# Kernel optimization log

Hardware: AMD Instinct MI355X
Metric: run time of the kernel (lower is better)

Reference implementation:

```python
import jax, jax.numpy as jnp
import numpy as np
import math

# --- config (matches init_kwargs) ---
C = 128          # sphere_channels (multiplicity per l)
LMAX = 2
H = 8            # attention heads
B = 16           # graphs per batch (uniform)
M = 512          # nodes per graph
N = B * M        # 8192 nodes
E = 262144       # edges
D = C * sum(2 * l + 1 for l in range(LMAX + 1))  # 1152
_INV_SQRT_C = 1.0 / math.sqrt(C)


def irreps_linear(x, W):
    """e3nn o3.Linear irreps_node->irreps_node: per-l channel mixing, shared over m.
    x: [N, D], W: [LMAX+1, C, C]."""
    outs = []
    s = 0
    for l in range(LMAX + 1):
        d = 2 * l + 1
        blk = x[:, s:s + C * d].reshape(-1, C, d)          # [N, C, 2l+1]
        y = jnp.einsum('ncm,oc->nom', blk, W[l]) * _INV_SQRT_C
        outs.append(y.reshape(-1, C * d))
        s += C * d
    return jnp.concatenate(outs, axis=1)


def init_edge_rot_mat(edge_vec, edge_rand):
    """Faithful port of init_edge_rot_mat; edge_rand plays the role of rand_like."""
    dist = jnp.sqrt(jnp.sum(edge_vec ** 2, axis=1, keepdims=True))
    nx_ = edge_vec / dist
    e2 = edge_rand - 0.5
    e2 = e2 / jnp.sqrt(jnp.sum(e2 ** 2, axis=1, keepdims=True))
    e2b = jnp.stack([-e2[:, 1], e2[:, 0], e2[:, 2]], axis=1)
    e2c = jnp.stack([e2[:, 0], -e2[:, 2], e2[:, 1]], axis=1)
    dot = lambda a: jnp.abs(jnp.sum(a * nx_, axis=1, keepdims=True))
    vdb, vdc = dot(e2b), dot(e2c)
    e2 = jnp.where(dot(e2) > vdb, e2b, e2)
    e2 = jnp.where(dot(e2) > vdc, e2c, e2)
    nz = jnp.cross(nx_, e2)
    nz = nz / jnp.sqrt(jnp.sum(nz ** 2, axis=1, keepdims=True))
    ny = jnp.cross(nx_, nz)
    ny = ny / jnp.sqrt(jnp.sum(ny ** 2, axis=1, keepdims=True))
    rot_inv = jnp.stack([nz, nx_, -ny], axis=2)  # columns [z, x, -y]
    return jnp.transpose(rot_inv, (0, 2, 1))     # [E, 3, 3]


def setup_inputs() -> dict:
    key = jax.random.key(0)
    ks = jax.random.split(key, 10)
    node_features = jax.random.normal(ks[0], (N, D), dtype=jnp.float32)
    edge_vec = jax.random.normal(ks[1], (E, 3), dtype=jnp.float32)
    edge_rand = jax.random.uniform(ks[2], (E, 3), dtype=jnp.float32)
    edge_index = jax.random.randint(ks[3], (2, E), 0, N, dtype=jnp.int32)
    batch = jnp.repeat(jnp.arange(B, dtype=jnp.int32), M)
    W_q = jax.random.normal(ks[4], (LMAX + 1, C, C), dtype=jnp.float32)
    W_k = jax.random.normal(ks[5], (LMAX + 1, C, C), dtype=jnp.float32)
    W_v = jax.random.normal(ks[6], (LMAX + 1, C, C), dtype=jnp.float32)
    W_o = jax.random.normal(ks[7], (LMAX + 1, C, C), dtype=jnp.float32)
    gamma = jnp.ones((C,), dtype=jnp.float32)
    beta = jnp.zeros((C,), dtype=jnp.float32)
    return dict(node_features=node_features, edge_vec=edge_vec, edge_rand=edge_rand,
                W_q=W_q, W_k=W_k, W_v=W_v, W_o=W_o, gamma=gamma, beta=beta,
                edge_index=edge_index, batch=batch)


def reference(node_features, edge_vec, edge_rand, W_q, W_k, W_v, W_o, gamma, beta,
              edge_index, batch):
    # 1) per-edge rotation matrices (detached in the original)
    rot = jax.lax.stop_gradient(init_edge_rot_mat(edge_vec, edge_rand))

    x = node_features  # [N, D] equivariant irreps features

    # 2) SO2EquivariantGraphAttention: irreps q/k/v, dense per-graph multi-head attn
    q = irreps_linear(x, W_q)
    k = irreps_linear(x, W_k)
    v = irreps_linear(x, W_v)
    hd = D // H
    scale = 1.0 / math.sqrt(hd)
    # to_dense_batch with uniform graph sizes == reshape; mask all-true
    qd = q.reshape(B, M, H, hd).transpose(0, 2, 1, 3)  # [B,H,M,hd]
    kd = k.reshape(B, M, H, hd).transpose(0, 2, 1, 3)
    vd = v.reshape(B, M, H, hd).transpose(0, 2, 1, 3)
    scores = jnp.einsum('bhqd,bhkd->bhqk', qd, kd) * scale
    attn_w = jax.nn.softmax(scores, axis=-1)
    o = jnp.einsum('bhqk,bhkd->bhqd', attn_w, vd)
    o = o.transpose(0, 2, 1, 3).reshape(N, D)
    attn_out = irreps_linear(o, W_o)

    # residual connection
    x = x + attn_out

    # 3) EquivariantLayerNormV2: LayerNorm over l=0 dims only (first C)
    inv = x[:, :C]
    mu = jnp.mean(inv, axis=-1, keepdims=True)
    var = jnp.var(inv, axis=-1, keepdims=True)
    inv = (inv - mu) / jnp.sqrt(var + 1e-5) * gamma + beta

    # 4) S2Activation: SiLU on scalar (l=0) components, identity elsewhere
    inv = jax.nn.silu(inv)
    out = jnp.concatenate([inv, x[:, C:]], axis=1)
    return out, rot
```

## Files before the change

kernel.cpp:

```cpp
#include <hip/hip_runtime.h>
#include <hip/hip_bf16.h>

#define C_CH   128
#define DROW   1152
#define NNODE  8192
#define BATCH  16
#define MSEQ   512
#define NHEAD  8
#define HD     144
#define NEDGE  262144

typedef unsigned short ushort_t;
typedef __attribute__((ext_vector_type(8))) short bf16x8;
typedef __attribute__((ext_vector_type(4))) float f32x4;

__device__ __forceinline__ float ldf(const float* p) { return *p; }
__device__ __forceinline__ float ldf(const __hip_bfloat16* p) { return __bfloat162float(*p); }
__device__ __forceinline__ ushort_t f2bu(float x) {
    __hip_bfloat16 h = __float2bfloat16(x);
    return *reinterpret_cast<ushort_t*>(&h);
}
__device__ __forceinline__ float bu2f(ushort_t u) {
    return __bfloat162float(*reinterpret_cast<__hip_bfloat16*>(&u));
}

#define KP2 136

template<int DL, int NPB, int NZ, int FUSE_LN, typename TX, typename TY>
__global__ __launch_bounds__(256) void lin_mfma(
    const TX* __restrict__ X,
    const float* __restrict__ W0, const float* __restrict__ W1,
    const float* __restrict__ W2,
    TY* __restrict__ Y0, TY* __restrict__ Y1, TY* __restrict__ Y2,
    const float* __restrict__ resid,
    const float* __restrict__ gamma, const float* __restrict__ beta,
    int baseoff)
{
    constexpr int COLS = NPB * DL;
    constexpr int CT   = COLS / 16;
    __shared__ __align__(16) ushort_t Xs[COLS][KP2];
    __shared__ __align__(16) ushort_t Es[COLS][KP2];

    const int tid  = threadIdx.x;
    const int wave = tid >> 6;
    const int lane = tid & 63;
    const int l15  = lane & 15;
    const int quad = lane >> 4;
    const int n0   = blockIdx.x * NPB;

    if constexpr (sizeof(TX) == 4) {
        for (int e4 = tid; e4 < NPB * 32 * DL; e4 += 256) {
            const int nb = e4 / (32 * DL);
            const int rr = (e4 - nb * (32 * DL)) * 4;
            const float4 xv = *reinterpret_cast<const float4*>(
                &X[(size_t)(n0 + nb) * DROW + baseoff + rr]);
            #pragma unroll
            for (int j = 0; j < 4; ++j) {
                const int r = rr + j, c = r / DL, m = r - c * DL;
                Xs[nb * DL + m][c] = f2bu(reinterpret_cast<const float*>(&xv)[j]);
            }
        }
    } else {
        for (int e8 = tid; e8 < NPB * 16 * DL; e8 += 256) {
            const int nb = e8 / (16 * DL);
            const int rr = (e8 - nb * (16 * DL)) * 8;
            const uint4 xv = *reinterpret_cast<const uint4*>(
                &X[(size_t)(n0 + nb) * DROW + baseoff + rr]);
            const ushort_t* xs = reinterpret_cast<const ushort_t*>(&xv);
            #pragma unroll
            for (int j = 0; j < 8; ++j) {
                const int r = rr + j, c = r / DL, m = r - c * DL;
                Xs[nb * DL + m][c] = xs[j];
            }
        }
    }

    const float s = 0.08838834764831845f;

    for (int z = 0; z < NZ; ++z) {
        const float* W = (z == 0) ? W0 : (z == 1 ? W1 : W2);
        TY* Y          = (z == 0) ? Y0 : (z == 1 ? Y1 : Y2);

        bf16x8 aw[2][4];
        #pragma unroll
        for (int ot = 0; ot < 2; ++ot)
            #pragma unroll
            for (int kst = 0; kst < 4; ++kst) {
                const float* wp = &W[(size_t)(32 * wave + 16 * ot + l15) * 128 + kst * 32 + quad * 8];
                const float4 wa = *reinterpret_cast<const float4*>(wp);
                const float4 wb = *reinterpret_cast<const float4*>(wp + 4);
                ushort_t t[8] = {f2bu(wa.x), f2bu(wa.y), f2bu(wa.z), f2bu(wa.w),
                                 f2bu(wb.x), f2bu(wb.y), f2bu(wb.z), f2bu(wb.w)};
                aw[ot][kst] = *reinterpret_cast<const bf16x8*>(t);
            }

        __syncthreads();

        f32x4 acc[CT][2];
        #pragma unroll
        for (int ct = 0; ct < CT; ++ct) {
            acc[ct][0] = (f32x4){0.f, 0.f, 0.f, 0.f};
            acc[ct][1] = (f32x4){0.f, 0.f, 0.f, 0.f};
        }
        #pragma unroll
        for (int kst = 0; kst < 4; ++kst)
            #pragma unroll
            for (int ct = 0; ct < CT; ++ct) {
                const bf16x8 b = *reinterpret_cast<const bf16x8*>(
                    &Xs[ct * 16 + l15][kst * 32 + quad * 8]);
                acc[ct][0] = __builtin_amdgcn_mfma_f32_16x16x32_bf16(aw[0][kst], b, acc[ct][0], 0, 0, 0);
                acc[ct][1] = __builtin_amdgcn_mfma_f32_16x16x32_bf16(aw[1][kst], b, acc[ct][1], 0, 0, 0);
            }

        #pragma unroll
        for (int ct = 0; ct < CT; ++ct)
            #pragma unroll
            for (int ot = 0; ot < 2; ++ot) {
                ushort_t t[4] = {f2bu(acc[ct][ot][0] * s), f2bu(acc[ct][ot][1] * s),
                                 f2bu(acc[ct][ot][2] * s), f2bu(acc[ct][ot][3] * s)};
                *reinterpret_cast<uint2*>(&Es[ct * 16 + l15][32 * wave + 16 * ot + quad * 4]) =
                    *reinterpret_cast<const uint2*>(t);
            }
        __syncthreads();

        if constexpr (FUSE_LN) {
            const int nb = tid >> 2, cc = tid & 3;
            float y[32];
            const float* xr = resid + (size_t)(n0 + nb) * DROW + cc * 32;
            float s1 = 0.f, s2 = 0.f;
            #pragma unroll
            for (int j4 = 0; j4 < 8; ++j4) {
                const float4 rv = *reinterpret_cast<const float4*>(xr + j4 * 4);
                #pragma unroll
                for (int j = 0; j < 4; ++j) {
                    const float v = bu2f(Es[nb][cc * 32 + j4 * 4 + j]) +
                                    reinterpret_cast<const float*>(&rv)[j];
                    y[j4 * 4 + j] = v; s1 += v; s2 += v * v;
                }
            }
            s1 += __shfl_xor(s1, 1); s2 += __shfl_xor(s2, 1);
            s1 += __shfl_xor(s1, 2); s2 += __shfl_xor(s2, 2);
            const float mean = s1 * (1.0f / 128.0f);
            const float var  = s2 * (1.0f / 128.0f) - mean * mean;
            const float rstd = rsqrtf(var + 1e-5f);
            float* op = (float*)Y + (size_t)(n0 + nb) * DROW + cc * 32;
            #pragma unroll
            for (int j4 = 0; j4 < 8; ++j4) {
                float4 ov;
                #pragma unroll
                for (int j = 0; j < 4; ++j) {
                    const int c = cc * 32 + j4 * 4 + j;
                    float t = (y[j4 * 4 + j] - mean) * rstd * gamma[c] + beta[c];
                    reinterpret_cast<float*>(&ov)[j] = t / (1.0f + __expf(-t));
                }
                *reinterpret_cast<float4*>(op + j4 * 4) = ov;
            }
        } else {
            for (int e8 = tid; e8 < COLS * 16; e8 += 256) {
                const int nb = e8 / (16 * DL);
                const int r0 = (e8 - nb * (16 * DL)) * 8;
                const size_t ga = (size_t)(n0 + nb) * DROW + baseoff + r0;
                if constexpr (sizeof(TY) == 2) {
                    ushort_t t[8];
                    #pragma unroll
                    for (int j = 0; j < 8; ++j) {
                        const int r = r0 + j;
                        t[j] = Es[nb * DL + r % DL][r / DL];
                    }
                    *reinterpret_cast<uint4*>(&Y[ga]) = *reinterpret_cast<const uint4*>(t);
                } else {
                    #pragma unroll
                    for (int j4 = 0; j4 < 2; ++j4) {
                        const float4 rv = *reinterpret_cast<const float4*>(&resid[ga + j4 * 4]);
                        float4 ov;
                        #pragma unroll
                        for (int j = 0; j < 4; ++j) {
                            const int r = r0 + j4 * 4 + j;
                            reinterpret_cast<float*>(&ov)[j] =
                                bu2f(Es[nb * DL + r % DL][r / DL]) +
                                reinterpret_cast<const float*>(&rv)[j];
                        }
                        *reinterpret_cast<float4*>(&((float*)Y)[ga + j4 * 4]) = ov;
                    }
                }
            }
        }
    }
}

#define KPAD  168
#define VROWS 160
#define VPAD2 72
#define PPAD  68

__global__ __launch_bounds__(256) void attn_kernel(
    const __hip_bfloat16* __restrict__ Q, const __hip_bfloat16* __restrict__ K,
    const __hip_bfloat16* __restrict__ V, __hip_bfloat16* __restrict__ O)
{
    __shared__ __align__(16) ushort_t ksqs[64][KPAD];
    __shared__ __align__(16) ushort_t vst[VROWS][VPAD2];
    __shared__ __align__(16) ushort_t ps[128][PPAD];

    const int tid  = threadIdx.x;
    const int wave = tid >> 6;
    const int lane = tid & 63;
    const int l15  = lane & 15;
    const int quad = lane >> 4;

    const int bid = blockIdx.x;
    const int xcd = bid & 7;
    const int j   = bid >> 3;
    const int bh  = xcd * 16 + (j >> 2);
    const int q0  = (j & 3) * 128;
    const int h   = bh & 7;
    const int b   = bh >> 3;
    const size_t rowbase = (size_t)b * MSEQ * DROW + (size_t)h * HD;
    const float EXSCALE = 0.12022458674074695f;

    for (int idx = tid; idx < 64 * 16; idx += 256)
        ksqs[idx >> 4][HD + (idx & 15)] = 0;
    for (int idx = tid; idx < 16 * VPAD2; idx += 256)
        vst[144 + idx / VPAD2][idx % VPAD2] = (idx / VPAD2 == 0) ? (ushort_t)0x3F80 : (ushort_t)0;

    bf16x8 aq[2][5];
    for (int hh = 0; hh < 2; ++hh) {
        __syncthreads();
        for (int idx = tid; idx < 64 * 18; idx += 256) {
            const int r = idx / 18, g = idx % 18;
            *reinterpret_cast<uint4*>(&ksqs[r][g * 8]) =
                *reinterpret_cast<const uint4*>(&Q[rowbase + (size_t)(q0 + hh * 64 + r) * DROW + g * 8]);
        }
        __syncthreads();
        if ((wave >> 1) == hh) {
            #pragma unroll
            for (int rt = 0; rt < 2; ++rt)
                #pragma unroll
                for (int kst = 0; kst < 5; ++kst)
                    aq[rt][kst] = *reinterpret_cast<const bf16x8*>(
                        &ksqs[32 * (wave & 1) + rt * 16 + l15][kst * 32 + quad * 8]);
        }
    }

    f32x4 oacc[2][10];
    #pragma unroll
    for (int rt = 0; rt < 2; ++rt)
        #pragma unroll
        for (int nt = 0; nt < 10; ++nt) oacc[rt][nt] = (f32x4){0.f, 0.f, 0.f, 0.f};

    for (int kc = 0; kc < 8; ++kc) {
        __syncthreads();
        for (int idx = tid; idx < 64 * 18; idx += 256) {
            const int r = idx / 18, g = idx % 18;
            *reinterpret_cast<uint4*>(&ksqs[r][g * 8]) =
                *reinterpret_cast<const uint4*>(&K[rowbase + (size_t)(kc * 64 + r) * DROW + g * 8]);
        }
        for (int it = tid; it < 16 * 18; it += 256) {
            const int rq = it / 18, g = it % 18;
            const size_t ga = rowbase + (size_t)(kc * 64 + rq * 4) * DROW + g * 8;
            const uint4 w0 = *reinterpret_cast<const uint4*>(&V[ga]);
            const uint4 w1 = *reinterpret_cast<const uint4*>(&V[ga + DROW]);
            const uint4 w2 = *reinterpret_cast<const uint4*>(&V[ga + 2 * DROW]);
            const uint4 w3 = *reinterpret_cast<const uint4*>(&V[ga + 3 * DROW]);
            const ushort_t* v0 = reinterpret_cast<const ushort_t*>(&w0);
            const ushort_t* v1 = reinterpret_cast<const ushort_t*>(&w1);
            const ushort_t* v2 = reinterpret_cast<const ushort_t*>(&w2);
            const ushort_t* v3 = reinterpret_cast<const ushort_t*>(&w3);
            #pragma unroll
            for (int i = 0; i < 8; ++i) {
                const int ii = (i + g + rq) & 7;
                uint2 pk;
                pk.x = (unsigned)v0[ii] | ((unsigned)v1[ii] << 16);
                pk.y = (unsigned)v2[ii] | ((unsigned)v3[ii] << 16);
                *reinterpret_cast<uint2*>(&vst[g * 8 + ii][rq * 4]) = pk;
            }
        }
        __syncthreads();

        f32x4 sc[2][4];
        #pragma unroll
        for (int rt = 0; rt < 2; ++rt)
            #pragma unroll
            for (int kt = 0; kt < 4; ++kt) sc[rt][kt] = (f32x4){0.f, 0.f, 0.f, 0.f};
        #pragma unroll
        for (int kst = 0; kst < 5; ++kst) {
            bf16x8 bk[4];
            #pragma unroll
            for (int kt = 0; kt < 4; ++kt)
                bk[kt] = *reinterpret_cast<const bf16x8*>(
                    &ksqs[kt * 16 + l15][kst * 32 + quad * 8]);
            #pragma unroll
            for (int rt = 0; rt < 2; ++rt)
                #pragma unroll
                for (int kt = 0; kt < 4; ++kt)
                    sc[rt][kt] = __builtin_amdgcn_mfma_f32_16x16x32_bf16(aq[rt][kst], bk[kt], sc[rt][kt], 0, 0, 0);
        }

        #pragma unroll
        for (int rt = 0; rt < 2; ++rt)
            #pragma unroll
            for (int kt = 0; kt < 4; ++kt)
                #pragma unroll
                for (int i = 0; i < 4; ++i)
                    ps[32 * wave + 16 * rt + quad * 4 + i][16 * kt + l15] =
                        f2bu(exp2f(sc[rt][kt][i] * EXSCALE));

        #pragma unroll
        for (int kp = 0; kp < 2; ++kp) {
            bf16x8 pa[2];
            #pragma unroll
            for (int rt = 0; rt < 2; ++rt)
                pa[rt] = *reinterpret_cast<const bf16x8*>(
                    &ps[32 * wave + 16 * rt + l15][kp * 32 + quad * 8]);
            #pragma unroll
            for (int nt = 0; nt < 10; ++nt) {
                const bf16x8 bv = *reinterpret_cast<const bf16x8*>(
                    &vst[nt * 16 + l15][kp * 32 + quad * 8]);
                #pragma unroll
                for (int rt = 0; rt < 2; ++rt)
                    oacc[rt][nt] = __builtin_amdgcn_mfma_f32_16x16x32_bf16(pa[rt], bv, oacc[rt][nt], 0, 0, 0);
            }
        }
    }

    #pragma unroll
    for (int rt = 0; rt < 2; ++rt) {
        #pragma unroll
        for (int i = 0; i < 4; ++i) {
            const float l = __shfl(oacc[rt][9][i], lane & 48);
            const float inv = 1.0f / l;
            const int row = q0 + 32 * wave + 16 * rt + quad * 4 + i;
            const size_t rb = rowbase + (size_t)row * DROW;
            #pragma unroll
            for (int nt = 0; nt < 9; ++nt)
                O[rb + nt * 16 + l15] = __float2bfloat16(oacc[rt][nt][i] * inv);
        }
    }
}

__global__ __launch_bounds__(256) void rot_kernel(
    const float* __restrict__ ev, const float* __restrict__ er,
    float* __restrict__ rot)
{
    const int e = blockIdx.x * 256 + threadIdx.x;
    if (e >= NEDGE) return;
    const float vx = ev[e * 3 + 0], vy = ev[e * 3 + 1], vz = ev[e * 3 + 2];
    const float d = sqrtf(vx * vx + vy * vy + vz * vz);
    const float nx0 = vx / d, nx1 = vy / d, nx2 = vz / d;
    float r0 = er[e * 3 + 0] - 0.5f;
    float r1 = er[e * 3 + 1] - 0.5f;
    float r2 = er[e * 3 + 2] - 0.5f;
    const float rn = sqrtf(r0 * r0 + r1 * r1 + r2 * r2);
    r0 /= rn; r1 /= rn; r2 /= rn;
    const float b0 = -r1, b1 = r0, b2v = r2;
    const float c0 = r0, c1 = -r2, c2 = r1;
    const float vd0 = fabsf(r0 * nx0 + r1 * nx1 + r2 * nx2);
    const float vdb = fabsf(b0 * nx0 + b1 * nx1 + b2v * nx2);
    const float vdc = fabsf(c0 * nx0 + c1 * nx1 + c2 * nx2);
    if (vd0 > vdb) { r0 = b0; r1 = b1; r2 = b2v; }
    const float vd1 = fabsf(r0 * nx0 + r1 * nx1 + r2 * nx2);
    if (vd1 > vdc) { r0 = c0; r1 = c1; r2 = c2; }
    float z0 = nx1 * r2 - nx2 * r1;
    float z1 = nx2 * r0 - nx0 * r2;
    float z2 = nx0 * r1 - nx1 * r0;
    const float zn = sqrtf(z0 * z0 + z1 * z1 + z2 * z2);
    z0 /= zn; z1 /= zn; z2 /= zn;
    float y0 = nx1 * z2 - nx2 * z1;
    float y1 = nx2 * z0 - nx0 * z2;
    float y2 = nx0 * z1 - nx1 * z0;
    const float yn = sqrtf(y0 * y0 + y1 * y1 + y2 * y2);
    y0 /= yn; y1 /= yn; y2 /= yn;
    float* rp = rot + (size_t)e * 9;
    rp[0] = z0;   rp[1] = z1;   rp[2] = z2;
    rp[3] = nx0;  rp[4] = nx1;  rp[5] = nx2;
    rp[6] = -y0;  rp[7] = -y1;  rp[8] = -y2;
}

extern "C" void kernel_launch(void* const* d_in, const int* in_sizes, int n_in,
                              void* d_out, int out_size, void* d_ws, size_t ws_size,
                              hipStream_t stream)
{
    (void)in_sizes; (void)n_in; (void)out_size; (void)ws_size;
    const float* x     = (const float*)d_in[0];
    const float* ev    = (const float*)d_in[1];
    const float* er    = (const float*)d_in[2];
    const float* Wq    = (const float*)d_in[3];
    const float* Wk    = (const float*)d_in[4];
    const float* Wv    = (const float*)d_in[5];
    const float* Wo    = (const float*)d_in[6];
    const float* gamma = (const float*)d_in[7];
    const float* beta  = (const float*)d_in[8];

    float* out = (float*)d_out;
    float* rot = out + (size_t)NNODE * DROW;

    const size_t ND = (size_t)NNODE * DROW;
    __hip_bfloat16* q = (__hip_bfloat16*)d_ws;
    __hip_bfloat16* k = q + ND;
    __hip_bfloat16* v = k + ND;
    __hip_bfloat16* o = v + ND;

    rot_kernel<<<NEDGE / 256, 256, 0, stream>>>(ev, er, rot);

    lin_mfma<1, 64, 3, 0, float, __hip_bfloat16><<<NNODE / 64, 256, 0, stream>>>(
        x, Wq, Wk, Wv, q, k, v, nullptr, nullptr, nullptr, 0);
    lin_mfma<3, 32, 3, 0, float, __hip_bfloat16><<<NNODE / 32, 256, 0, stream>>>(
        x, Wq + 16384, Wk + 16384, Wv + 16384, q, k, v, nullptr, nullptr, nullptr, 128);
    lin_mfma<5, 16, 3, 0, float, __hip_bfloat16><<<NNODE / 16, 256, 0, stream>>>(
        x, Wq + 32768, Wk + 32768, Wv + 32768, q, k, v, nullptr, nullptr, nullptr, 512);

    attn_kernel<<<(MSEQ / 128) * NHEAD * BATCH, 256, 0, stream>>>(q, k, v, o);

    lin_mfma<1, 64, 1, 1, __hip_bfloat16, float><<<NNODE / 64, 256, 0, stream>>>(
        o, Wo, nullptr, nullptr, out, nullptr, nullptr, x, gamma, beta, 0);
    lin_mfma<3, 32, 1, 0, __hip_bfloat16, float><<<NNODE / 32, 256, 0, stream>>>(
        o, Wo + 16384, nullptr, nullptr, out, nullptr, nullptr, x, nullptr, nullptr, 128);
    lin_mfma<5, 16, 1, 0, __hip_bfloat16, float><<<NNODE / 16, 256, 0, stream>>>(
        o, Wo + 32768, nullptr, nullptr, out, nullptr, nullptr, x, nullptr, nullptr, 512);
}
```

Before: 272.2 us.

## Prefetch next K/V tile into registers to overlap loads with attention compute

The attention kernel now loads the next K and V chunk from global memory into registers right after the shared-memory tiles are written, so the loads are in flight while the current chunk's QK and PV MFMAs run. The first chunk's load is issued before the Q staging. Launch bounds also ask for two blocks per CU, which caps register use. The prefetch buffers add about 52 VGPRs on top of the existing accumulators, so spills or lower occupancy are possible.

Result: no change. 268.6 us (-1.3%).

```diff
diff --git a/kernel.cpp b/kernel.cpp
--- a/kernel.cpp
+++ b/kernel.cpp
@@ -193,7 +193,7 @@
 #define VPAD2 72
 #define PPAD  68
 
-__global__ __launch_bounds__(256) void attn_kernel(
+__global__ __launch_bounds__(256, 2) void attn_kernel(
     const __hip_bfloat16* __restrict__ Q, const __hip_bfloat16* __restrict__ K,
     const __hip_bfloat16* __restrict__ V, __hip_bfloat16* __restrict__ O)
 {
@@ -217,54 +217,58 @@
     const size_t rowbase = (size_t)b * MSEQ * DROW + (size_t)h * HD;
     const float EXSCALE = 0.12022458674074695f;
 
-    for (int idx = tid; idx < 64 * 16; idx += 256)
-        ksqs[idx >> 4][HD + (idx & 15)] = 0;
-    for (int idx = tid; idx < 16 * VPAD2; idx += 256)
-        vst[144 + idx / VPAD2][idx % VPAD2] = (idx / VPAD2 == 0) ? (ushort_t)0x3F80 : (ushort_t)0;
-
-    bf16x8 aq[2][5];
-    for (int hh = 0; hh < 2; ++hh) {
-        __syncthreads();
-        for (int idx = tid; idx < 64 * 18; idx += 256) {
+    uint4 kpre[5];
+    uint4 vpre[2][4];
+
+    auto load_kv = [&](int kc) {
+        #pragma unroll
+        for (int s = 0; s < 4; ++s) {
+            const int idx = tid + s * 256;
             const int r = idx / 18, g = idx % 18;
-            *reinterpret_cast<uint4*>(&ksqs[r][g * 8]) =
-                *reinterpret_cast<const uint4*>(&Q[rowbase + (size_t)(q0 + hh * 64 + r) * DROW + g * 8]);
-        }
-        __syncthreads();
-        if ((wave >> 1) == hh) {
-            #pragma unroll
-            for (int rt = 0; rt < 2; ++rt)
-                #pragma unroll
-                for (int kst = 0; kst < 5; ++kst)
-                    aq[rt][kst] = *reinterpret_cast<const bf16x8*>(
-                        &ksqs[32 * (wave & 1) + rt * 16 + l15][kst * 32 + quad * 8]);
-        }
-    }
-
-    f32x4 oacc[2][10];
-    #pragma unroll
-    for (int rt = 0; rt < 2; ++rt)
-        #pragma unroll
-        for (int nt = 0; nt < 10; ++nt) oacc[rt][nt] = (f32x4){0.f, 0.f, 0.f, 0.f};
-
-    for (int kc = 0; kc < 8; ++kc) {
-        __syncthreads();
-        for (int idx = tid; idx < 64 * 18; idx += 256) {
+            kpre[s] = *reinterpret_cast<const uint4*>(
+                &K[rowbase + (size_t)(kc * 64 + r) * DROW + g * 8]);
+        }
+        if (tid < 128) {
+            const int idx = tid + 1024;
             const int r = idx / 18, g = idx % 18;
-            *reinterpret_cast<uint4*>(&ksqs[r][g * 8]) =
-                *reinterpret_cast<const uint4*>(&K[rowbase + (size_t)(kc * 64 + r) * DROW + g * 8]);
-        }
-        for (int it = tid; it < 16 * 18; it += 256) {
+            kpre[4] = *reinterpret_cast<const uint4*>(
+                &K[rowbase + (size_t)(kc * 64 + r) * DROW + g * 8]);
+        }
+        {
+            const int rq = tid / 18, g = tid % 18;
+            const size_t ga = rowbase + (size_t)(kc * 64 + rq * 4) * DROW + g * 8;
+            #pragma unroll
+            for (int w = 0; w < 4; ++w)
+                vpre[0][w] = *reinterpret_cast<const uint4*>(&V[ga + (size_t)w * DROW]);
+        }
+        if (tid < 32) {
+            const int it = tid + 256;
             const int rq = it / 18, g = it % 18;
             const size_t ga = rowbase + (size_t)(kc * 64 + rq * 4) * DROW + g * 8;
-            const uint4 w0 = *reinterpret_cast<const uint4*>(&V[ga]);
-            const uint4 w1 = *reinterpret_cast<const uint4*>(&V[ga + DROW]);
-            const uint4 w2 = *reinterpret_cast<const uint4*>(&V[ga + 2 * DROW]);
-            const uint4 w3 = *reinterpret_cast<const uint4*>(&V[ga + 3 * DROW]);
-            const ushort_t* v0 = reinterpret_cast<const ushort_t*>(&w0);
-            const ushort_t* v1 = reinterpret_cast<const ushort_t*>(&w1);
-            const ushort_t* v2 = reinterpret_cast<const ushort_t*>(&w2);
-            const ushort_t* v3 = reinterpret_cast<const ushort_t*>(&w3);
+            #pragma unroll
+            for (int w = 0; w < 4; ++w)
+                vpre[1][w] = *reinterpret_cast<const uint4*>(&V[ga + (size_t)w * DROW]);
+        }
+    };
+
+    auto write_kv = [&]() {
+        #pragma unroll
+        for (int s = 0; s < 4; ++s) {
+            const int idx = tid + s * 256;
+            const int r = idx / 18, g = idx % 18;
+            *reinterpret_cast<uint4*>(&ksqs[r][g * 8]) = kpre[s];
+        }
+        if (tid < 128) {
+            const int idx = tid + 1024;
+            const int r = idx / 18, g = idx % 18;
+            *reinterpret_cast<uint4*>(&ksqs[r][g * 8]) = kpre[4];
+        }
+        {
+            const int rq = tid / 18, g = tid % 18;
+            const ushort_t* v0 = reinterpret_cast<const ushort_t*>(&vpre[0][0]);
+            const ushort_t* v1 = reinterpret_cast<const ushort_t*>(&vpre[0][1]);
+            const ushort_t* v2 = reinterpret_cast<const ushort_t*>(&vpre[0][2]);
+            const ushort_t* v3 = reinterpret_cast<const ushort_t*>(&vpre[0][3]);
             #pragma unroll
             for (int i = 0; i < 8; ++i) {
                 const int ii = (i + g + rq) & 7;
@@ -274,7 +278,61 @@
                 *reinterpret_cast<uint2*>(&vst[g * 8 + ii][rq * 4]) = pk;
             }
         }
-        __syncthreads();
+        if (tid < 32) {
+            const int it = tid + 256;
+            const int rq = it / 18, g = it % 18;
+            const ushort_t* v0 = reinterpret_cast<const ushort_t*>(&vpre[1][0]);
+            const ushort_t* v1 = reinterpret_cast<const ushort_t*>(&vpre[1][1]);
+            const ushort_t* v2 = reinterpret_cast<const ushort_t*>(&vpre[1][2]);
+            const ushort_t* v3 = reinterpret_cast<const ushort_t*>(&vpre[1][3]);
+            #pragma unroll
+            for (int i = 0; i < 8; ++i) {
+                const int ii = (i + g + rq) & 7;
+                uint2 pk;
+                pk.x = (unsigned)v0[ii] | ((unsigned)v1[ii] << 16);
+                pk.y = (unsigned)v2[ii] | ((unsigned)v3[ii] << 16);
+                *reinterpret_cast<uint2*>(&vst[g * 8 + ii][rq * 4]) = pk;
+            }
+        }
+    };
+
+    load_kv(0);
+
+    for (int idx = tid; idx < 64 * 16; idx += 256)
+        ksqs[idx >> 4][HD + (idx & 15)] = 0;
+    for (int idx = tid; idx < 16 * VPAD2; idx += 256)
+        vst[144 + idx / VPAD2][idx % VPAD2] = (idx / VPAD2 == 0) ? (ushort_t)0x3F80 : (ushort_t)0;
+
+    bf16x8 aq[2][5];
+    for (int hh = 0; hh < 2; ++hh) {
+        __syncthreads();
+        for (int idx = tid; idx < 64 * 18; idx += 256) {
+            const int r = idx / 18, g = idx % 18;
+            *reinterpret_cast<uint4*>(&ksqs[r][g * 8]) =
+                *reinterpret_cast<const uint4*>(&Q[rowbase + (size_t)(q0 + hh * 64 + r) * DROW + g * 8]);
+        }
+        __syncthreads();
+        if ((wave >> 1) == hh) {
+            #pragma unroll
+            for (int rt = 0; rt < 2; ++rt)
+                #pragma unroll
+                for (int kst = 0; kst < 5; ++kst)
+                    aq[rt][kst] = *reinterpret_cast<const bf16x8*>(
+                        &ksqs[32 * (wave & 1) + rt * 16 + l15][kst * 32 + quad * 8]);
+        }
+    }
+
+    f32x4 oacc[2][10];
+    #pragma unroll
+    for (int rt = 0; rt < 2; ++rt)
+        #pragma unroll
+        for (int nt = 0; nt < 10; ++nt) oacc[rt][nt] = (f32x4){0.f, 0.f, 0.f, 0.f};
+
+    for (int kc = 0; kc < 8; ++kc) {
+        __syncthreads();
+        write_kv();
+        __syncthreads();
+        if (kc < 7) load_kv(kc + 1);
 
         f32x4 sc[2][4];
         #pragma unroll
```

## Prefetch next K/V tiles into registers during attention compute

Applied to the files above, without the earlier changes.

The attention kernel now issues the global loads for the next 64-row K and V chunk into registers while the current chunk's QK and PV MFMA work runs. The registers are written to LDS at the start of the next iteration, which hides global memory latency behind compute. Launch bounds now request two blocks per SM, which caps register use. The prefetch adds many live registers, so spilling or lower occupancy is a risk. The V transpose loses its rotated index order, which may add LDS bank conflicts.

New measurement: 244.3 us. 1.11x faster.

```diff
diff --git a/kernel.cpp b/kernel.cpp
--- a/kernel.cpp
+++ b/kernel.cpp
@@ -22,6 +22,11 @@
 }
 __device__ __forceinline__ float bu2f(ushort_t u) {
     return __bfloat162float(*reinterpret_cast<__hip_bfloat16*>(&u));
+}
+__device__ __forceinline__ unsigned u16of(const uint4 v, int ii) {
+    const unsigned w = ((ii >> 1) == 0) ? v.x : ((ii >> 1) == 1) ? v.y :
+                       ((ii >> 1) == 2) ? v.z : v.w;
+    return (ii & 1) ? (w >> 16) : (w & 0xFFFFu);
 }
 
 #define KP2 136
@@ -193,7 +198,7 @@
 #define VPAD2 72
 #define PPAD  68
 
-__global__ __launch_bounds__(256) void attn_kernel(
+__global__ __launch_bounds__(256, 2) void attn_kernel(
     const __hip_bfloat16* __restrict__ Q, const __hip_bfloat16* __restrict__ K,
     const __hip_bfloat16* __restrict__ V, __hip_bfloat16* __restrict__ O)
 {
@@ -217,6 +222,79 @@
     const size_t rowbase = (size_t)b * MSEQ * DROW + (size_t)h * HD;
     const float EXSCALE = 0.12022458674074695f;
 
+    const int r0 = tid / 18,          g0 = tid % 18;
+    const int r1 = (tid + 256) / 18,  g1 = (tid + 256) % 18;
+    const int r2 = (tid + 512) / 18,  g2 = (tid + 512) % 18;
+    const int r3 = (tid + 768) / 18,  g3 = (tid + 768) % 18;
+    const int r4 = (tid + 1024) / 18, g4 = (tid + 1024) % 18;
+    const int ko0 = r0 * DROW + g0 * 8, ko1 = r1 * DROW + g1 * 8;
+    const int ko2 = r2 * DROW + g2 * 8, ko3 = r3 * DROW + g3 * 8;
+    const int ko4 = r4 * DROW + g4 * 8;
+    ushort_t* kld0 = &ksqs[r0][g0 * 8];
+    ushort_t* kld1 = &ksqs[r1][g1 * 8];
+    ushort_t* kld2 = &ksqs[r2][g2 * 8];
+    ushort_t* kld3 = &ksqs[r3][g3 * 8];
+    ushort_t* kld4 = &ksqs[r4][g4 * 8];
+    const int rqa = tid / 18,          ga = tid % 18;
+    const int rqb = (tid + 256) / 18,  gb = (tid + 256) % 18;
+    const int voa = (rqa * 4) * DROW + ga * 8;
+    const int vob = (rqb * 4) * DROW + gb * 8;
+    const bool hasK4 = (tid < 128);
+    const bool hasVB = (tid < 32);
+
+    uint4 kp0, kp1, kp2, kp3, kp4;
+    uint4 va0, va1, va2, va3, vb0, vb1, vb2, vb3;
+
+#define LOAD_K(KC) do { \
+        const __hip_bfloat16* kb_ = K + rowbase + (size_t)((KC) * 64) * DROW; \
+        kp0 = *reinterpret_cast<const uint4*>(kb_ + ko0); \
+        kp1 = *reinterpret_cast<const uint4*>(kb_ + ko1); \
+        kp2 = *reinterpret_cast<const uint4*>(kb_ + ko2); \
+        kp3 = *reinterpret_cast<const uint4*>(kb_ + ko3); \
+        if (hasK4) kp4 = *reinterpret_cast<const uint4*>(kb_ + ko4); \
+    } while (0)
+
+#define LOAD_V(KC) do { \
+        const __hip_bfloat16* vbp_ = V + rowbase + (size_t)((KC) * 64) * DROW; \
+        va0 = *reinterpret_cast<const uint4*>(vbp_ + voa); \
+        va1 = *reinterpret_cast<const uint4*>(vbp_ + voa + DROW); \
+        va2 = *reinterpret_cast<const uint4*>(vbp_ + voa + 2 * DROW); \
+        va3 = *reinterpret_cast<const uint4*>(vbp_ + voa + 3 * DROW); \
+        if (hasVB) { \
+            vb0 = *reinterpret_cast<const uint4*>(vbp_ + vob); \
+            vb1 = *reinterpret_cast<const uint4*>(vbp_ + vob + DROW); \
+            vb2 = *reinterpret_cast<const uint4*>(vbp_ + vob + 2 * DROW); \
+            vb3 = *reinterpret_cast<const uint4*>(vbp_ + vob + 3 * DROW); \
+        } \
+    } while (0)
+
+#define WRITE_KV() do { \
+        *reinterpret_cast<uint4*>(kld0) = kp0; \
+        *reinterpret_cast<uint4*>(kld1) = kp1; \
+        *reinterpret_cast<uint4*>(kld2) = kp2; \
+        *reinterpret_cast<uint4*>(kld3) = kp3; \
+        if (hasK4) *reinterpret_cast<uint4*>(kld4) = kp4; \
+        _Pragma("unroll") \
+        for (int ii = 0; ii < 8; ++ii) { \
+            uint2 pk; \
+            pk.x = u16of(va0, ii) | (u16of(va1, ii) << 16); \
+            pk.y = u16of(va2, ii) | (u16of(va3, ii) << 16); \
+            *reinterpret_cast<uint2*>(&vst[ga * 8 + ii][rqa * 4]) = pk; \
+        } \
+        if (hasVB) { \
+            _Pragma("unroll") \
+            for (int ii = 0; ii < 8; ++ii) { \
+                uint2 pk; \
+                pk.x = u16of(vb0, ii) | (u16of(vb1, ii) << 16); \
+                pk.y = u16of(vb2, ii) | (u16of(vb3, ii) << 16); \
+                *reinterpret_cast<uint2*>(&vst[gb * 8 + ii][rqb * 4]) = pk; \
+            } \
+        } \
+    } while (0)
+
+    LOAD_K(0);
+    LOAD_V(0);
+
     for (int idx = tid; idx < 64 * 16; idx += 256)
         ksqs[idx >> 4][HD + (idx & 15)] = 0;
     for (int idx = tid; idx < 16 * VPAD2; idx += 256)
@@ -249,32 +327,9 @@
 
     for (int kc = 0; kc < 8; ++kc) {
         __syncthreads();
-        for (int idx = tid; idx < 64 * 18; idx += 256) {
-            const int r = idx / 18, g = idx % 18;
-            *reinterpret_cast<uint4*>(&ksqs[r][g * 8]) =
-                *reinterpret_cast<const uint4*>(&K[rowbase + (size_t)(kc * 64 + r) * DROW + g * 8]);
-        }
-        for (int it = tid; it < 16 * 18; it += 256) {
-            const int rq = it / 18, g = it % 18;
-            const size_t ga = rowbase + (size_t)(kc * 64 + rq * 4) * DROW + g * 8;
-            const uint4 w0 = *reinterpret_cast<const uint4*>(&V[ga]);
-            const uint4 w1 = *reinterpret_cast<const uint4*>(&V[ga + DROW]);
-            const uint4 w2 = *reinterpret_cast<const uint4*>(&V[ga + 2 * DROW]);
-            const uint4 w3 = *reinterpret_cast<const uint4*>(&V[ga + 3 * DROW]);
-            const ushort_t* v0 = reinterpret_cast<const ushort_t*>(&w0);
-            const ushort_t* v1 = reinterpret_cast<const ushort_t*>(&w1);
-            const ushort_t* v2 = reinterpret_cast<const ushort_t*>(&w2);
-            const ushort_t* v3 = reinterpret_cast<const ushort_t*>(&w3);
-            #pragma unroll
-            for (int i = 0; i < 8; ++i) {
-                const int ii = (i + g + rq) & 7;
-                uint2 pk;
-                pk.x = (unsigned)v0[ii] | ((unsigned)v1[ii] << 16);
-                pk.y = (unsigned)v2[ii] | ((unsigned)v3[ii] << 16);
-                *reinterpret_cast<uint2*>(&vst[g * 8 + ii][rq * 4]) = pk;
-            }
-        }
-        __syncthreads();
+        WRITE_KV();
+        __syncthreads();
+        if (kc < 7) LOAD_K(kc + 1);
 
         f32x4 sc[2][4];
         #pragma unroll
@@ -294,6 +349,8 @@
                 for (int kt = 0; kt < 4; ++kt)
                     sc[rt][kt] = __builtin_amdgcn_mfma_f32_16x16x32_bf16(aq[rt][kst], bk[kt], sc[rt][kt], 0, 0, 0);
         }
+
+        if (kc < 7) LOAD_V(kc + 1);
 
         #pragma unroll
         for (int rt = 0; rt < 2; ++rt)
@@ -335,6 +392,9 @@
                 O[rb + nt * 16 + l15] = __float2bfloat16(oacc[rt][nt][i] * inv);
         }
     }
+#undef LOAD_K
+#undef LOAD_V
+#undef WRITE_KV
 }
 
 __global__ __launch_bounds__(256) void rot_kernel(
```
